# Kernel optimization log

Measured on AMD Instinct MI355X. Metric: run time of the kernel, lower is better.

The kernel has to match this reference:

```python
import jax, jax.numpy as jnp
import numpy as np
import math

DIM = 1024
NUM_HEADS = 16


def setup_inputs() -> dict:
    key = jax.random.key(0)
    ks = jax.random.split(key, 6)
    B, S, D = 2, 2048, DIM
    return {
        "q": jax.random.normal(ks[0], (B, S, D), dtype=jnp.float32),
        "k": jax.random.normal(ks[1], (B, S, D), dtype=jnp.float32),
        "v": jax.random.normal(ks[2], (B, S, D), dtype=jnp.float32),
        "wq": jax.random.normal(ks[3], (D, D), dtype=jnp.float32),
        "wk": jax.random.normal(ks[4], (D, D), dtype=jnp.float32),
        "wv": jax.random.normal(ks[5], (D, D), dtype=jnp.float32),
    }


def reference(q, k, v, wq, wk, wv):
    B, S, D = q.shape
    H = NUM_HEADS
    hd = D // H
    # projections: [B,S,D] @ [D,D]
    qp = (q @ wq).reshape(B, H, S, hd)  # NOTE: direct reshape, as in the original
    kp = (k @ wk).reshape(B, H, S, hd)
    vp = (v @ wv).reshape(B, H, S, hd)
    scale = 1.0 / math.sqrt(D)  # original scales by sqrt(dim), not sqrt(head_dim)
    att = jnp.einsum("bhqd,bhkd->bhqk", qp, kp) * scale  # [B,H,S,S]
    att = jax.nn.softmax(att, axis=-1)
    out = jnp.einsum("bhqk,bhkd->bhqd", att, vp)  # [B,H,S,hd]
    out = out.transpose(0, 2, 1, 3).reshape(B, S, D)
    return out
```

## Files before the change

### kernel.cpp

```cpp
#include <hip/hip_runtime.h>
#include <hip/hip_bf16.h>
#include <stdint.h>

#define DIMD 1024
#define SEQ  2048
#define NH   16
#define MROWS 4096
#define NQ   65536

typedef __bf16 bf16_t;
typedef bf16_t bf16x8 __attribute__((ext_vector_type(8)));
typedef float  f32x4  __attribute__((ext_vector_type(4)));
typedef unsigned short u16;
typedef unsigned short u16x4 __attribute__((ext_vector_type(4)));
typedef unsigned short u16x8 __attribute__((ext_vector_type(8)));
typedef unsigned int   u32;
typedef u32 u32x2 __attribute__((ext_vector_type(2)));

static __device__ __forceinline__ f32x4 mfma16(bf16x8 a, bf16x8 b, f32x4 c) {
    return __builtin_amdgcn_mfma_f32_16x16x32_bf16(a, b, c, 0, 0, 0);
}

static __device__ __forceinline__ float fast_exp2(float x) {
#if __has_builtin(__builtin_amdgcn_exp2f)
    return __builtin_amdgcn_exp2f(x);
#else
    return exp2f(x);
#endif
}

#define GLD16(gsrc, ldst) __builtin_amdgcn_global_load_lds(                    \
    (const __attribute__((address_space(1))) unsigned int*)(gsrc),             \
    (__attribute__((address_space(3))) unsigned int*)(ldst), 16, 0, 0)

static __device__ __forceinline__ void split_bf16(float x, u16& h, u16& l) {
    u32 u = __float_as_uint(x);
    u16 hu = (u16)(u >> 16);
    float xh = __uint_as_float((u32)hu << 16);
    float lo = x - xh;
    h = hu;
    l = (u16)(__float_as_uint(lo) >> 16);
}

static __device__ __forceinline__ u32 pack_bf16(float a, float b) {
    return (__float_as_uint(a) >> 16) | (__float_as_uint(b) & 0xffff0000u);
}
static __device__ __forceinline__ u32 pack_bf16_rn(float a, float b) {
    u32 ua = __float_as_uint(a) + 0x8000u;
    u32 ub = __float_as_uint(b) + 0x8000u;
    return (ua >> 16) | (ub & 0xffff0000u);
}
static __device__ __forceinline__ float bf_to_f(u16 v) {
    return __uint_as_float((u32)v << 16);
}

__global__ __launch_bounds__(256) void transWs3(
    const float* __restrict__ w0, const float* __restrict__ w1, const float* __restrict__ w2,
    u16* __restrict__ WTsH, u16* __restrict__ WTsL) {
    const int z = blockIdx.z;
    const float* W = z == 0 ? w0 : z == 1 ? w1 : w2;
    __shared__ u16 Hs[4096], Ls[4096];
    const int tid = threadIdx.x;
    const int kt = blockIdx.x, nt = blockIdx.y;
    const int n0 = nt * 128, k0 = kt * 32;
    #pragma unroll
    for (int i = 0; i < 4; i++) {
        int f = i * 256 + tid;
        int kr = f >> 5, nc4 = (f & 31) * 4;
        f32x4 w = *(const f32x4*)&W[(size_t)(k0 + kr) * DIMD + n0 + nc4];
        int cc = kr >> 3, e = kr & 7;
        #pragma unroll
        for (int j = 0; j < 4; j++) {
            u16 hh, ll; split_bf16(w[j], hh, ll);
            Hs[cc * 1024 + (nc4 + j) * 8 + e] = hh;
            Ls[cc * 1024 + (nc4 + j) * 8 + e] = ll;
        }
    }
    __syncthreads();
    const size_t base = (size_t)z * (DIMD * DIMD) + (size_t)(nt * 32 + kt) * 4096;
    #pragma unroll
    for (int i = 0; i < 2; i++) {
        int idx = (i * 256 + tid) * 8;
        *(u16x8*)(WTsH + base + idx) = *(const u16x8*)&Hs[idx];
        *(u16x8*)(WTsL + base + idx) = *(const u16x8*)&Ls[idx];
    }
}

__global__ __launch_bounds__(256, 3) void proj7(
    const float* __restrict__ xq, const float* __restrict__ xk, const float* __restrict__ xv,
    const u16* __restrict__ WTsH, const u16* __restrict__ WTsL,
    u16* __restrict__ qh, u16* __restrict__ ql,
    u16* __restrict__ kh, u16* __restrict__ kl,
    u16* __restrict__ vh) {

    const int z = blockIdx.z;
    const float* X = z == 0 ? xq : z == 1 ? xk : xv;
    const u16* BH = WTsH + (size_t)z * (DIMD * DIMD);
    const u16* BL = WTsL + (size_t)z * (DIMD * DIMD);
    u16* outH = z == 0 ? qh : z == 1 ? kh : vh;
    u16* outL = z == 0 ? ql : kl;
    const float oscale = z == 0 ? 0.0450842200278f : 1.0f;

    __shared__ u16 lds[24576];
    u16* AsH = lds;
    u16* AsL = lds + 4096;

    const int tid  = threadIdx.x;
    const int lane = tid & 63, wave = tid >> 6;
    const int quad = lane >> 4, l16 = lane & 15;
    const int wy = wave >> 1, wx = wave & 1;
    const int m0 = blockIdx.x * 128;
    const int n0 = blockIdx.y * 128;
    const size_t Bregion0 = (size_t)(blockIdx.y * 32) * 4096;

    const int rA  = tid >> 2, ccA = tid & 3;
    const int idxA0 = ccA * 1024 + ((rA ^ (ccA << 1)) * 8);
    const int idxA1 = idxA0 + 512;
    const float* Xb0 = X + (size_t)(m0 + rA) * DIMD + ccA * 8;
    const float* Xb1 = X + (size_t)(m0 + rA + 64) * DIMD + ccA * 8;

    f32x4 acc[4][4];
    #pragma unroll
    for (int mt = 0; mt < 4; mt++)
        #pragma unroll
        for (int nt = 0; nt < 4; nt++) acc[mt][nt] = (f32x4)0.0f;

    f32x4 pa0, pa1, pa2, pa3;

#define LOADA(kt) do {                                                         \
        pa0 = *(const f32x4*)(Xb0 + (kt) * 32);                                \
        pa1 = *(const f32x4*)(Xb0 + (kt) * 32 + 4);                            \
        pa2 = *(const f32x4*)(Xb1 + (kt) * 32);                                \
        pa3 = *(const f32x4*)(Xb1 + (kt) * 32 + 4);                            \
    } while (0)

#define WRITEA() do {                                                          \
        u16x8 h, l;                                                            \
        _Pragma("unroll")                                                      \
        for (int j = 0; j < 4; j++) {                                          \
            u16 hh, ll;                                                        \
            split_bf16(pa0[j], hh, ll); h[j] = hh;     l[j] = ll;              \
            split_bf16(pa1[j], hh, ll); h[4 + j] = hh; l[4 + j] = ll;          \
        }                                                                      \
        *(u16x8*)&AsH[idxA0] = h;                                              \
        *(u16x8*)&AsL[idxA0] = l;                                              \
        _Pragma("unroll")                                                      \
        for (int j = 0; j < 4; j++) {                                          \
            u16 hh, ll;                                                        \
            split_bf16(pa2[j], hh, ll); h[j] = hh;     l[j] = ll;              \
            split_bf16(pa3[j], hh, ll); h[4 + j] = hh; l[4 + j] = ll;          \
        }                                                                      \
        *(u16x8*)&AsH[idxA1] = h;                                              \
        *(u16x8*)&AsL[idxA1] = l;                                              \
    } while (0)

#define STAGEB(kt, buf) do {                                                   \
        const size_t rb = Bregion0 + (size_t)(kt) * 4096;                      \
        u16* BsHd = lds + 8192 + (buf) * 8192;                                 \
        u16* BsLd = BsHd + 4096;                                               \
        int c0 = tid, c1 = 256 + tid;                                          \
        GLD16(BH + rb + c0 * 8, &BsHd[c0 * 8]);                                \
        GLD16(BH + rb + c1 * 8, &BsHd[c1 * 8]);                                \
        GLD16(BL + rb + c0 * 8, &BsLd[c0 * 8]);                                \
        GLD16(BL + rb + c1 * 8, &BsLd[c1 * 8]);                                \
    } while (0)

    LOADA(0);
    STAGEB(0, 0);
    WRITEA();
    __syncthreads();

    for (int kt = 0; kt < 32; kt++) {
        const int cur = kt & 1;
        if (kt < 31) {
            LOADA(kt + 1);
            STAGEB(kt + 1, cur ^ 1);
        }

        const u16* BsH = lds + 8192 + cur * 8192;
        const u16* BsL = BsH + 4096;

        bf16x8 aH[4], aL[4], bH[4], bL[4];
        #pragma unroll
        for (int mt = 0; mt < 4; mt++) {
            int r = wy * 64 + mt * 16 + l16;
            int idx = quad * 1024 + ((r ^ (quad << 1)) * 8);
            aH[mt] = *(const bf16x8*)&AsH[idx];
            aL[mt] = *(const bf16x8*)&AsL[idx];
        }
        #pragma unroll
        for (int nt = 0; nt < 4; nt++) {
            int r = wx * 64 + nt * 16 + l16;
            bH[nt] = *(const bf16x8*)&BsH[(quad * 128 + r) * 8];
            bL[nt] = *(const bf16x8*)&BsL[(quad * 128 + r) * 8];
        }
        #pragma unroll
        for (int mt = 0; mt < 4; mt++)
            #pragma unroll
            for (int nt = 0; nt < 4; nt++) {
                acc[mt][nt] = mfma16(aH[mt], bH[nt], acc[mt][nt]);
                acc[mt][nt] = mfma16(aH[mt], bL[nt], acc[mt][nt]);
                acc[mt][nt] = mfma16(aL[mt], bH[nt], acc[mt][nt]);
            }

        __syncthreads();
        if (kt < 31) WRITEA();
        __syncthreads();
    }
#undef LOADA
#undef WRITEA
#undef STAGEB

    #pragma unroll
    for (int mt = 0; mt < 4; mt++)
        #pragma unroll
        for (int nt = 0; nt < 4; nt++)
            #pragma unroll
            for (int r = 0; r < 4; r++) {
                int row = m0 + wy * 64 + mt * 16 + quad * 4 + r;
                int col = n0 + wx * 64 + nt * 16 + l16;
                u16 hh, ll; split_bf16(acc[mt][nt][r] * oscale, hh, ll);
                outH[(size_t)row * DIMD + col] = hh;
                if (z != 2) outL[(size_t)row * DIMD + col] = ll;
            }
}

__global__ __launch_bounds__(256) void transposeV(
    const u16* __restrict__ vh, u16* __restrict__ vt) {
    __shared__ u16 Ls[64][72];
    const int tid = threadIdx.x;
    const int bh = blockIdx.y;
    const int s0 = blockIdx.x * 64;
    const size_t slab = (size_t)bh * (SEQ * 64);
    #pragma unroll
    for (int i = 0; i < 2; i++) {
        int f = i * 256 + tid;
        int r = f >> 3, c = (f & 7) * 8;
        *(u16x8*)&Ls[r][c] = *(const u16x8*)(vh + slab + (size_t)(s0 + r) * 64 + c);
    }
    __syncthreads();
    #pragma unroll
    for (int i = 0; i < 2; i++) {
        int f = i * 256 + tid;
        int d = f >> 3, j = (f & 7) * 8;
        u16x8 o;
        #pragma unroll
        for (int jj = 0; jj < 8; jj++) o[jj] = Ls[j + jj][d];
        *(u16x8*)(vt + slab + (size_t)d * SEQ + s0 + j) = o;
    }
}

__global__ __launch_bounds__(256, 3) void flash6(
    const u16* __restrict__ qh, const u16* __restrict__ ql,
    const u16* __restrict__ kh, const u16* __restrict__ kl,
    const u16* __restrict__ vt,
    u16* __restrict__ Opart, float* __restrict__ Mpart, float* __restrict__ Lpart) {

    __shared__ u16 KH[64][72], KL[64][72], VTs[64][72];
    __shared__ u16 Ps[4][32][72];

    const int tid  = threadIdx.x;
    const int lane = tid & 63, wv = tid >> 6;
    const int quad = lane >> 4, l16 = lane & 15;
    const int bh = blockIdx.x, z = blockIdx.z;
    const size_t slab = (size_t)bh * (SEQ * 64);
    const int q0 = blockIdx.y * 128 + wv * 32;
    const int jbase = z * 1024;

    bf16x8 qfH[2][2], qfL[2][2];
    #pragma unroll
    for (int mq = 0; mq < 2; mq++) {
        const size_t rb = slab + (size_t)(q0 + mq * 16 + l16) * 64;
        #pragma unroll
        for (int kk = 0; kk < 2; kk++) {
            qfH[mq][kk] = *(const bf16x8*)(qh + rb + kk * 32 + quad * 8);
            qfL[mq][kk] = *(const bf16x8*)(ql + rb + kk * 32 + quad * 8);
        }
    }

    f32x4 O[2][4];
    float M[2] = {-3.0e38f, -3.0e38f}, L[2] = {0.0f, 0.0f};
    #pragma unroll
    for (int mq = 0; mq < 2; mq++)
        #pragma unroll
        for (int nv = 0; nv < 4; nv++) O[mq][nv] = (f32x4)0.0f;

    const int f0 = tid, f1 = 256 + tid;
    const int r0 = f0 >> 3, c0 = (f0 & 7) * 8;
    const int r1 = f1 >> 3, c1 = (f1 & 7) * 8;
    u16x8 s0, s1, s2, s3, s4, s5;

    {
        const int j0 = jbase;
        s0 = *(const u16x8*)(kh + slab + (size_t)(j0 + r0) * 64 + c0);
        s1 = *(const u16x8*)(kh + slab + (size_t)(j0 + r1) * 64 + c1);
        s2 = *(const u16x8*)(kl + slab + (size_t)(j0 + r0) * 64 + c0);
        s3 = *(const u16x8*)(kl + slab + (size_t)(j0 + r1) * 64 + c1);
        s4 = *(const u16x8*)(vt + slab + (size_t)r0 * SEQ + j0 + c0);
        s5 = *(const u16x8*)(vt + slab + (size_t)r1 * SEQ + j0 + c1);
    }
    *(u16x8*)&KH[r0][c0] = s0;  *(u16x8*)&KH[r1][c1] = s1;
    *(u16x8*)&KL[r0][c0] = s2;  *(u16x8*)&KL[r1][c1] = s3;
    *(u16x8*)&VTs[r0][c0] = s4; *(u16x8*)&VTs[r1][c1] = s5;
    __syncthreads();

    for (int t = 0; t < 16; t++) {
        if (t < 15) {
            const int j0 = jbase + (t + 1) * 64;
            s0 = *(const u16x8*)(kh + slab + (size_t)(j0 + r0) * 64 + c0);
            s1 = *(const u16x8*)(kh + slab + (size_t)(j0 + r1) * 64 + c1);
            s2 = *(const u16x8*)(kl + slab + (size_t)(j0 + r0) * 64 + c0);
            s3 = *(const u16x8*)(kl + slab + (size_t)(j0 + r1) * 64 + c1);
            s4 = *(const u16x8*)(vt + slab + (size_t)r0 * SEQ + j0 + c0);
            s5 = *(const u16x8*)(vt + slab + (size_t)r1 * SEQ + j0 + c1);
        }

        f32x4 St[2][4];
        #pragma unroll
        for (int mq = 0; mq < 2; mq++)
            #pragma unroll
            for (int nt = 0; nt < 4; nt++) St[mq][nt] = (f32x4)0.0f;
        __builtin_amdgcn_s_setprio(1);
        #pragma unroll
        for (int nt = 0; nt < 4; nt++) {
            const int rB = nt * 16 + l16;
            #pragma unroll
            for (int kk = 0; kk < 2; kk++) {
                bf16x8 kHf = *(const bf16x8*)&KH[rB][kk * 32 + quad * 8];
                bf16x8 kLf = *(const bf16x8*)&KL[rB][kk * 32 + quad * 8];
                #pragma unroll
                for (int mq = 0; mq < 2; mq++) {
                    St[mq][nt] = mfma16(kHf, qfH[mq][kk], St[mq][nt]);
                    St[mq][nt] = mfma16(kLf, qfH[mq][kk], St[mq][nt]);
                    St[mq][nt] = mfma16(kHf, qfL[mq][kk], St[mq][nt]);
                }
            }
        }
        __builtin_amdgcn_s_setprio(0);

        #pragma unroll
        for (int mq = 0; mq < 2; mq++) {
            float mx = St[mq][0][0];
            #pragma unroll
            for (int nt = 0; nt < 4; nt++)
                #pragma unroll
                for (int r = 0; r < 4; r++) mx = fmaxf(mx, St[mq][nt][r]);
            mx = fmaxf(mx, __shfl_xor(mx, 16));
            mx = fmaxf(mx, __shfl_xor(mx, 32));
            float Mn = M[mq];
            if (__any(mx > Mn)) {
                Mn = fmaxf(Mn, mx);
                float al = fast_exp2(M[mq] - Mn);
                M[mq] = Mn;
                L[mq] *= al;
                #pragma unroll
                for (int nv = 0; nv < 4; nv++) O[mq][nv] *= al;
            }
            float rs = 0.0f;
            #pragma unroll
            for (int nt = 0; nt < 4; nt++)
                #pragma unroll
                for (int r = 0; r < 4; r++) {
                    float p = fast_exp2(St[mq][nt][r] - Mn);
                    St[mq][nt][r] = p;
                    rs += p;
                }
            rs += __shfl_xor(rs, 16);
            rs += __shfl_xor(rs, 32);
            L[mq] += rs;
            #pragma unroll
            for (int nt = 0; nt < 4; nt++) {
                u32x2 d;
                d[0] = pack_bf16(St[mq][nt][0], St[mq][nt][1]);
                d[1] = pack_bf16(St[mq][nt][2], St[mq][nt][3]);
                *(u32x2*)&Ps[wv][mq * 16 + l16][nt * 16 + quad * 4] = d;
            }
        }

        __builtin_amdgcn_s_setprio(1);
        #pragma unroll
        for (int kk = 0; kk < 2; kk++) {
            bf16x8 pB[2];
            #pragma unroll
            for (int mq = 0; mq < 2; mq++)
                pB[mq] = *(const bf16x8*)&Ps[wv][mq * 16 + l16][kk * 32 + quad * 8];
            #pragma unroll
            for (int nv = 0; nv < 4; nv++) {
                bf16x8 vF = *(const bf16x8*)&VTs[nv * 16 + l16][kk * 32 + quad * 8];
                #pragma unroll
                for (int mq = 0; mq < 2; mq++)
                    O[mq][nv] = mfma16(vF, pB[mq], O[mq][nv]);
            }
        }
        __builtin_amdgcn_s_setprio(0);

        __syncthreads();
        if (t < 15) {
            *(u16x8*)&KH[r0][c0] = s0;  *(u16x8*)&KH[r1][c1] = s1;
            *(u16x8*)&KL[r0][c0] = s2;  *(u16x8*)&KL[r1][c1] = s3;
            *(u16x8*)&VTs[r0][c0] = s4; *(u16x8*)&VTs[r1][c1] = s5;
        }
        __syncthreads();
    }

    const int qgb = bh * SEQ + q0;
    #pragma unroll
    for (int mq = 0; mq < 2; mq++) {
        const int qg = qgb + mq * 16 + l16;
        #pragma unroll
        for (int nv = 0; nv < 4; nv++) {
            u32x2 d;
            d[0] = pack_bf16_rn(O[mq][nv][0], O[mq][nv][1]);
            d[1] = pack_bf16_rn(O[mq][nv][2], O[mq][nv][3]);
            *(u32x2*)(Opart + ((size_t)(z * NQ + qg)) * 64 + nv * 16 + quad * 4) = d;
        }
        if (quad == 0) {
            Mpart[z * NQ + qg] = M[mq];
            Lpart[z * NQ + qg] = L[mq];
        }
    }
}

__global__ __launch_bounds__(256) void combineK(
    const u16* __restrict__ Opart, const float* __restrict__ Mpart,
    const float* __restrict__ Lpart, float* __restrict__ out) {
    int idx = blockIdx.x * 256 + threadIdx.x;
    int qg = idx >> 4, c4 = (idx & 15) * 4;
    float M0 = Mpart[qg], M1 = Mpart[NQ + qg];
    float L0 = Lpart[qg], L1 = Lpart[NQ + qg];
    float Ms = fmaxf(M0, M1);
    float w0 = fast_exp2(M0 - Ms), w1 = fast_exp2(M1 - Ms);
    float inv = 1.0f / (w0 * L0 + w1 * L1);
    u16x4 a = *(const u16x4*)&Opart[(size_t)qg * 64 + c4];
    u16x4 b = *(const u16x4*)&Opart[((size_t)NQ + qg) * 64 + c4];
    f32x4 o;
    #pragma unroll
    for (int j = 0; j < 4; j++)
        o[j] = (w0 * bf_to_f(a[j]) + w1 * bf_to_f(b[j])) * inv;
    int bh = qg >> 11, s = qg & 2047;
    int bb = bh >> 4, h = bh & 15;
    *(f32x4*)&out[((size_t)(bb * SEQ + s)) * DIMD + h * 64 + c4] = o;
}

extern "C" void kernel_launch(void* const* d_in, const int* in_sizes, int n_in,
                              void* d_out, int out_size, void* d_ws, size_t ws_size,
                              hipStream_t stream) {
    const float* q  = (const float*)d_in[0];
    const float* k  = (const float*)d_in[1];
    const float* v  = (const float*)d_in[2];
    const float* wq = (const float*)d_in[3];
    const float* wk = (const float*)d_in[4];
    const float* wv = (const float*)d_in[5];
    float* out = (float*)d_out;

    char* ws = (char*)d_ws;
    const size_t MB = 1 << 20;
    u16* qh   = (u16*)(ws + 0 * MB);
    u16* ql   = (u16*)(ws + 8 * MB);
    u16* kh   = (u16*)(ws + 16 * MB);
    u16* kl   = (u16*)(ws + 24 * MB);
    u16* vh   = (u16*)(ws + 32 * MB);
    u16* vt   = (u16*)(ws + 40 * MB);
    u16* WTsH = (u16*)(ws + 48 * MB);
    u16* WTsL = (u16*)(ws + 54 * MB);
    u16*   Opart = (u16*)(ws + 48 * MB);
    float* Mpart = (float*)(ws + 64 * MB);
    float* Lpart = (float*)(ws + 64 * MB + 512 * 1024);

    transWs3<<<dim3(32, 8, 3), 256, 0, stream>>>(wq, wk, wv, WTsH, WTsL);

    proj7<<<dim3(32, 8, 3), 256, 0, stream>>>(
        q, k, v, WTsH, WTsL, qh, ql, kh, kl, vh);

    transposeV<<<dim3(SEQ / 64, 2 * NH), 256, 0, stream>>>(vh, vt);

    flash6<<<dim3(2 * NH, SEQ / 128, 2), 256, 0, stream>>>(
        qh, ql, kh, kl, vt, Opart, Mpart, Lpart);

    combineK<<<dim3(NQ * 16 / 256), 256, 0, stream>>>(Opart, Mpart, Lpart, out);
}
```

Measured before the change: 265.8 us.

## Drop split-K flash attention and combine kernel; swizzle V transpose LDS

The flash kernel no longer splits the key dimension into two halves with a separate combine pass. Each block now walks all 2048 keys and normalises and writes fp32 output directly. This removes the bf16 partial-output round trip, the M/L buffers and one kernel launch, but halves the grid to 512 blocks, so fewer waves are in flight on a large GPU. The V transpose also XOR-swizzles its LDS columns to cut bank conflicts on the column-wise reads.

```diff
diff --git a/kernel.cpp b/kernel.cpp
--- a/kernel.cpp
+++ b/kernel.cpp
@@ -44,14 +44,6 @@
 
 static __device__ __forceinline__ u32 pack_bf16(float a, float b) {
     return (__float_as_uint(a) >> 16) | (__float_as_uint(b) & 0xffff0000u);
-}
-static __device__ __forceinline__ u32 pack_bf16_rn(float a, float b) {
-    u32 ua = __float_as_uint(a) + 0x8000u;
-    u32 ub = __float_as_uint(b) + 0x8000u;
-    return (ua >> 16) | (ub & 0xffff0000u);
-}
-static __device__ __forceinline__ float bf_to_f(u16 v) {
-    return __uint_as_float((u32)v << 16);
 }
 
 __global__ __launch_bounds__(256) void transWs3(
@@ -236,7 +228,8 @@
     for (int i = 0; i < 2; i++) {
         int f = i * 256 + tid;
         int r = f >> 3, c = (f & 7) * 8;
-        *(u16x8*)&Ls[r][c] = *(const u16x8*)(vh + slab + (size_t)(s0 + r) * 64 + c);
+        int csw = c ^ (((r >> 3) & 7) << 3);
+        *(u16x8*)&Ls[r][csw] = *(const u16x8*)(vh + slab + (size_t)(s0 + r) * 64 + c);
     }
     __syncthreads();
     #pragma unroll
@@ -245,16 +238,18 @@
         int d = f >> 3, j = (f & 7) * 8;
         u16x8 o;
         #pragma unroll
-        for (int jj = 0; jj < 8; jj++) o[jj] = Ls[j + jj][d];
+        for (int jj = 0; jj < 8; jj++) {
+            int rr = j + jj;
+            o[jj] = Ls[rr][d ^ (((rr >> 3) & 7) << 3)];
+        }
         *(u16x8*)(vt + slab + (size_t)d * SEQ + s0 + j) = o;
     }
 }
 
-__global__ __launch_bounds__(256, 3) void flash6(
+__global__ __launch_bounds__(256, 3) void flash11(
     const u16* __restrict__ qh, const u16* __restrict__ ql,
     const u16* __restrict__ kh, const u16* __restrict__ kl,
-    const u16* __restrict__ vt,
-    u16* __restrict__ Opart, float* __restrict__ Mpart, float* __restrict__ Lpart) {
+    const u16* __restrict__ vt, float* __restrict__ out) {
 
     __shared__ u16 KH[64][72], KL[64][72], VTs[64][72];
     __shared__ u16 Ps[4][32][72];
@@ -262,10 +257,9 @@
     const int tid  = threadIdx.x;
     const int lane = tid & 63, wv = tid >> 6;
     const int quad = lane >> 4, l16 = lane & 15;
-    const int bh = blockIdx.x, z = blockIdx.z;
+    const int bh = blockIdx.x;
     const size_t slab = (size_t)bh * (SEQ * 64);
     const int q0 = blockIdx.y * 128 + wv * 32;
-    const int jbase = z * 1024;
 
     bf16x8 qfH[2][2], qfL[2][2];
     #pragma unroll
@@ -291,22 +285,21 @@
     u16x8 s0, s1, s2, s3, s4, s5;
 
     {
-        const int j0 = jbase;
-        s0 = *(const u16x8*)(kh + slab + (size_t)(j0 + r0) * 64 + c0);
-        s1 = *(const u16x8*)(kh + slab + (size_t)(j0 + r1) * 64 + c1);
-        s2 = *(const u16x8*)(kl + slab + (size_t)(j0 + r0) * 64 + c0);
-        s3 = *(const u16x8*)(kl + slab + (size_t)(j0 + r1) * 64 + c1);
-        s4 = *(const u16x8*)(vt + slab + (size_t)r0 * SEQ + j0 + c0);
-        s5 = *(const u16x8*)(vt + slab + (size_t)r1 * SEQ + j0 + c1);
+        s0 = *(const u16x8*)(kh + slab + (size_t)r0 * 64 + c0);
+        s1 = *(const u16x8*)(kh + slab + (size_t)r1 * 64 + c1);
+        s2 = *(const u16x8*)(kl + slab + (size_t)r0 * 64 + c0);
+        s3 = *(const u16x8*)(kl + slab + (size_t)r1 * 64 + c1);
+        s4 = *(const u16x8*)(vt + slab + (size_t)r0 * SEQ + c0);
+        s5 = *(const u16x8*)(vt + slab + (size_t)r1 * SEQ + c1);
     }
     *(u16x8*)&KH[r0][c0] = s0;  *(u16x8*)&KH[r1][c1] = s1;
     *(u16x8*)&KL[r0][c0] = s2;  *(u16x8*)&KL[r1][c1] = s3;
     *(u16x8*)&VTs[r0][c0] = s4; *(u16x8*)&VTs[r1][c1] = s5;
     __syncthreads();
 
-    for (int t = 0; t < 16; t++) {
-        if (t < 15) {
-            const int j0 = jbase + (t + 1) * 64;
+    for (int t = 0; t < 32; t++) {
+        if (t < 31) {
+            const int j0 = (t + 1) * 64;
             s0 = *(const u16x8*)(kh + slab + (size_t)(j0 + r0) * 64 + c0);
             s1 = *(const u16x8*)(kh + slab + (size_t)(j0 + r1) * 64 + c1);
             s2 = *(const u16x8*)(kl + slab + (size_t)(j0 + r0) * 64 + c0);
@@ -395,7 +388,7 @@
         __builtin_amdgcn_s_setprio(0);
 
         __syncthreads();
-        if (t < 15) {
+        if (t < 31) {
             *(u16x8*)&KH[r0][c0] = s0;  *(u16x8*)&KH[r1][c1] = s1;
             *(u16x8*)&KL[r0][c0] = s2;  *(u16x8*)&KL[r1][c1] = s3;
             *(u16x8*)&VTs[r0][c0] = s4; *(u16x8*)&VTs[r1][c1] = s5;
@@ -403,43 +396,20 @@
         __syncthreads();
     }
 
-    const int qgb = bh * SEQ + q0;
+    const int bb = bh >> 4, hh = bh & 15;
     #pragma unroll
     for (int mq = 0; mq < 2; mq++) {
-        const int qg = qgb + mq * 16 + l16;
+        const int s = q0 + mq * 16 + l16;
+        const float inv = 1.0f / L[mq];
+        float* orow = out + ((size_t)(bb * SEQ + s)) * DIMD + hh * 64;
         #pragma unroll
         for (int nv = 0; nv < 4; nv++) {
-            u32x2 d;
-            d[0] = pack_bf16_rn(O[mq][nv][0], O[mq][nv][1]);
-            d[1] = pack_bf16_rn(O[mq][nv][2], O[mq][nv][3]);
-            *(u32x2*)(Opart + ((size_t)(z * NQ + qg)) * 64 + nv * 16 + quad * 4) = d;
-        }
-        if (quad == 0) {
-            Mpart[z * NQ + qg] = M[mq];
-            Lpart[z * NQ + qg] = L[mq];
-        }
-    }
-}
-
-__global__ __launch_bounds__(256) void combineK(
-    const u16* __restrict__ Opart, const float* __restrict__ Mpart,
-    const float* __restrict__ Lpart, float* __restrict__ out) {
-    int idx = blockIdx.x * 256 + threadIdx.x;
-    int qg = idx >> 4, c4 = (idx & 15) * 4;
-    float M0 = Mpart[qg], M1 = Mpart[NQ + qg];
-    float L0 = Lpart[qg], L1 = Lpart[NQ + qg];
-    float Ms = fmaxf(M0, M1);
-    float w0 = fast_exp2(M0 - Ms), w1 = fast_exp2(M1 - Ms);
-    float inv = 1.0f / (w0 * L0 + w1 * L1);
-    u16x4 a = *(const u16x4*)&Opart[(size_t)qg * 64 + c4];
-    u16x4 b = *(const u16x4*)&Opart[((size_t)NQ + qg) * 64 + c4];
-    f32x4 o;
-    #pragma unroll
-    for (int j = 0; j < 4; j++)
-        o[j] = (w0 * bf_to_f(a[j]) + w1 * bf_to_f(b[j])) * inv;
-    int bh = qg >> 11, s = qg & 2047;
-    int bb = bh >> 4, h = bh & 15;
-    *(f32x4*)&out[((size_t)(bb * SEQ + s)) * DIMD + h * 64 + c4] = o;
+            f32x4 o4;
+            #pragma unroll
+            for (int r = 0; r < 4; r++) o4[r] = O[mq][nv][r] * inv;
+            *(f32x4*)(orow + nv * 16 + quad * 4) = o4;
+        }
+    }
 }
 
 extern "C" void kernel_launch(void* const* d_in, const int* in_sizes, int n_in,
@@ -463,9 +433,6 @@
     u16* vt   = (u16*)(ws + 40 * MB);
     u16* WTsH = (u16*)(ws + 48 * MB);
     u16* WTsL = (u16*)(ws + 54 * MB);
-    u16*   Opart = (u16*)(ws + 48 * MB);
-    float* Mpart = (float*)(ws + 64 * MB);
-    float* Lpart = (float*)(ws + 64 * MB + 512 * 1024);
 
     transWs3<<<dim3(32, 8, 3), 256, 0, stream>>>(wq, wk, wv, WTsH, WTsL);
 
@@ -474,8 +441,6 @@
 
     transposeV<<<dim3(SEQ / 64, 2 * NH), 256, 0, stream>>>(vh, vt);
 
-    flash6<<<dim3(2 * NH, SEQ / 128, 2), 256, 0, stream>>>(
-        qh, ql, kh, kl, vt, Opart, Mpart, Lpart);
-
-    combineK<<<dim3(NQ * 16 / 256), 256, 0, stream>>>(Opart, Mpart, Lpart, out);
-}
+    flash11<<<dim3(2 * NH, SEQ / 128), 256, 0, stream>>>(
+        qh, ql, kh, kl, vt, out);
+}
```

Measured after the change: 249.9 us. 1.06x faster.
